# Optimization experiments

Hardware: AMD Instinct MI355X
Metric: run time of the kernel (lower is better)

Reference implementation:

```python
import jax, jax.numpy as jnp
import numpy as np

# Fixed canonical tree batching: complete binary tree, depth D, 2^D - 1 internal nodes.
O, P_, D = 64, 64, 6          # num_obs, num_particles, tree depth
H, OBS, SD, AD = 100, 100, 8, 10  # hidden, obs_emb, sample_emb, address_emb dims
IN = OBS + SD + AD            # GRUCell input dim = 118
N = 2 ** D - 1                # internal nodes per tree


def setup_inputs() -> dict:
    key = jax.random.key(0)
    ks = jax.random.split(key, 13)
    f = lambda k, s: jax.random.normal(k, s, dtype=jnp.float32)
    return {
        "obs_embeddings": f(ks[0], (O, OBS)),
        "sample_emb": f(ks[1], (O, P_, N, SD)),
        "addr_emb": f(ks[2], (O, P_, N, AD)),
        "W_ih": f(ks[3], (3 * H, IN)) * 0.1,
        "W_hh": f(ks[4], (3 * H, H)) * 0.1,
        "b_ih": f(ks[5], (3 * H,)) * 0.1,
        "b_hh": f(ks[6], (3 * H,)) * 0.1,
        "W1": f(ks[7], (50, H)) * 0.1,
        "b1": f(ks[8], (50,)) * 0.1,
        "W2": f(ks[9], (25, 50)) * 0.1,
        "b2": f(ks[10], (25,)) * 0.1,
        "W3": f(ks[11], (1, 25)) * 0.1,
        "b3": f(ks[12], (1,)) * 0.1,
    }


def reference(obs_embeddings, sample_emb, addr_emb, W_ih, W_hh, b_ih, b_hh,
              W1, b1, W2, b2, W3, b3):
    def gru_cell(x, h):
        # torch.nn.GRUCell math
        gi = x @ W_ih.T + b_ih
        gh = h @ W_hh.T + b_hh
        i_r, i_z, i_n = jnp.split(gi, 3, axis=-1)
        h_r, h_z, h_n = jnp.split(gh, 3, axis=-1)
        r = jax.nn.sigmoid(i_r + h_r)
        z = jax.nn.sigmoid(i_z + h_z)
        n = jnp.tanh(i_n + r * h_n)
        return (1.0 - z) * n + z * h

    # Leaves (terminals) contribute zero hidden state, per the torch code.
    h_child = jnp.zeros((O, P_, 2 ** (D - 1), H), dtype=sample_emb.dtype)
    h = h_child
    # Bottom-up over levels (root = level 0). Level l has 2^l nodes,
    # occupying flat indices [2^l - 1, 2^(l+1) - 2].
    for l in range(D - 1, -1, -1):
        w = 2 ** l
        s = w - 1
        obs_b = jnp.broadcast_to(obs_embeddings[:, None, None, :], (O, P_, w, OBS))
        x = jnp.concatenate(
            [obs_b, sample_emb[:, :, s:s + w], addr_emb[:, :, s:s + w]], axis=-1)
        h = gru_cell(x, h_child)  # [O, P_, w, H]
        if l > 0:
            # Parent hidden input = sum of its two children's embeddings.
            h_child = h.reshape(O, P_, w // 2, 2, H).sum(axis=3)
    root = h[:, :, 0, :]  # [O, P_, H]
    y = jax.nn.relu(root @ W1.T + b1)
    y = jax.nn.relu(y @ W2.T + b2)
    c = (y @ W3.T + b3)[..., 0]  # [O, P_]
    return jax.nn.logsumexp(c, axis=1) - jnp.log(jnp.float32(P_))
```

## Files before the change

### kernel.cpp

```cpp
#include <hip/hip_runtime.h>
#include <hip/hip_bf16.h>

typedef __attribute__((ext_vector_type(8))) short bf16x8;
typedef __attribute__((ext_vector_type(4))) float f32x4;

__device__ __forceinline__ float sigmoidf_(float x){ return 1.0f/(1.0f+__expf(-x)); }
__device__ __forceinline__ float tanhf_(float x){ return 1.0f - 2.0f/(1.0f+__expf(2.0f*x)); }
__device__ __forceinline__ unsigned short f2bf(float f){
    __hip_bfloat16 b = __float2bfloat16(f);
    return *reinterpret_cast<unsigned short*>(&b);
}
__device__ __forceinline__ float bf2f(unsigned short u){
    __hip_bfloat16 b = *reinterpret_cast<__hip_bfloat16*>(&u);
    return __bfloat162float(b);
}
__device__ __forceinline__ void gload_lds16(const void* gsrc, void* ldst){
    __builtin_amdgcn_global_load_lds(
        (const __attribute__((address_space(1))) unsigned int*)gsrc,
        (__attribute__((address_space(3))) unsigned int*)ldst,
        16, 0, 0);
}

__global__ __launch_bounds__(64) void precompute_kernel(
    const float* __restrict__ obs, const float* __restrict__ W_ih,
    const float* __restrict__ W_hh, const float* __restrict__ b_ih,
    const float* __restrict__ b_hh, const float* __restrict__ W1,
    const float* __restrict__ W2,
    unsigned short* __restrict__ Bg,
    float* __restrict__ W1T, float* __restrict__ W2T)
{
    int t = blockIdx.x * 64 + threadIdx.x;
    if (t < 688128) {
        int o = t / 10752, r = t % 10752;
        int s = r / 512, r2 = r % 512;
        int j = r2 / 32, kk = r2 % 32;
        int region = s / 7;
        int u = (s % 7) * 16 + j;
        unsigned short outv = 0;
        if (u < 100) {
            int gate = region * 100 + u;
            if (kk < 18) {
                outv = f2bf(W_ih[(size_t)gate * 118 + 100 + kk]);
            } else if (kk == 18 || kk == 19) {
                float bias = b_ih[gate] + (region < 2 ? b_hh[gate] : 0.f);
                const float* orow = obs + o * 100;
                const float* wrow = W_ih + (size_t)gate * 118;
                for (int k = 0; k < 100; ++k) bias = fmaf(orow[k], wrow[k], bias);
                if (kk == 18) outv = f2bf(bias);
                else          outv = f2bf(bias - bf2f(f2bf(bias)));
            }
        }
        int qr = kk >> 3, e = kk & 7;
        Bg[(size_t)o * 10752 + (size_t)((s * 4 + qr) * 16 + j) * 8 + e] = outv;
        return;
    }
    t -= 688128;
    if (t < 43008) {
        int ks = 1 + t / 10752, r = t % 10752;
        int s = r / 512, r2 = r % 512;
        int j = r2 / 32, kk = r2 % 32;
        int tt = (s < 14) ? s : s + 7;
        int region = tt / 7;
        int u = (tt % 7) * 16 + j;
        float wv = 0.f;
        if (u < 100) {
            int gate = (region == 3 ? 2 : region) * 100 + u;
            int kh = (ks - 1) * 32 + kk;
            if (kh < 100) wv = W_hh[(size_t)gate * 100 + kh];
        }
        int qr = kk >> 3, e = kk & 7;
        Bg[(size_t)688128 + (size_t)(ks - 1) * 10752
           + (size_t)((s * 4 + qr) * 16 + j) * 8 + e] = f2bf(wv);
        return;
    }
    t -= 43008;
    if (t < 512) {
        Bg[731136 + t] = 0;
        return;
    }
    t -= 512;
    if (t < 5000) { int g = t / 50, j = t % 50; W1T[t] = W1[j * 100 + g]; return; }
    t -= 5000;
    if (t < 1250) { int j = t / 25, i = t % 25; W2T[t] = W2[i * 50 + j]; }
}

template<int LW1, bool LEAF1, bool LAST>
__global__ __launch_bounds__(512) void fused_pair(
    const unsigned short* __restrict__ Bg,
    const float* __restrict__ bhh,
    const float* __restrict__ samp,
    const float* __restrict__ addr,
    const unsigned short* __restrict__ hin,
    unsigned short* __restrict__ hout)
{
    extern __shared__ unsigned short smem[];
    unsigned short* B0   = smem;
    unsigned short* BH   = smem + 10752;
    unsigned short* hmid = smem + 54272;

    const int tid = threadIdx.x;
    const int lane = tid & 63;
    const int wid = tid >> 6;
    const int j15 = lane & 15;
    const int qr = lane >> 4;
    const int wk = (blockIdx.x & 7) * (gridDim.x >> 3) + (blockIdx.x >> 3);
    const int c0 = wk * 128;
    const int c0w = c0 + wid * 16;
    const int o = c0 >> (LW1 + 6);

    {
        const char* g0 = (const char*)(Bg + (size_t)o * 10752);
        const char* gH = (const char*)(Bg + 688128);
        char* l0 = (char*)smem;
        #pragma unroll
        for (int it = 0; it < 13; ++it) {
            const int base = it * 512 + wid * 64;
            const int fi = base + lane;
            const char* src = (fi < 1344) ? g0 + (size_t)fi * 16
                                          : gH + (size_t)(fi - 1344) * 16;
            gload_lds16(src, l0 + (size_t)base * 16);
        }
        if (wid < 2) {
            const int base = 6656 + wid * 64;
            const int fi = base + lane;
            gload_lds16(gH + (size_t)(fi - 1344) * 16, l0 + (size_t)base * 16);
        }
    }

    f32x4 acc[28];
    #pragma unroll
    for (int t = 0; t < 28; ++t) acc[t] = (f32x4){0.f, 0.f, 0.f, 0.f};

    bf16x8 axhi, axlo;
    {
        const int w = 1 << LW1;
        const int cm = c0w + j15;
        const int opm = cm >> LW1;
        const int nodem = w - 1 + (cm & (w - 1));
        const size_t nb = (size_t)opm * 63 + nodem;
        float xv0=0.f,xv1=0.f,xv2=0.f,xv3=0.f,xv4=0.f,xv5=0.f,xv6=0.f,xv7=0.f;
        if (qr == 0) {
            const float4* s4 = (const float4*)(samp + nb * 8);
            float4 a = s4[0], b = s4[1];
            xv0=a.x; xv1=a.y; xv2=a.z; xv3=a.w; xv4=b.x; xv5=b.y; xv6=b.z; xv7=b.w;
        } else if (qr == 1) {
            const float2* a2 = (const float2*)(addr + nb * 10);
            float2 e0=a2[0], e1=a2[1], e2=a2[2], e3=a2[3];
            xv0=e0.x; xv1=e0.y; xv2=e1.x; xv3=e1.y; xv4=e2.x; xv5=e2.y; xv6=e3.x; xv7=e3.y;
        } else if (qr == 2) {
            xv0 = addr[nb * 10 + 8]; xv1 = addr[nb * 10 + 9];
            xv2 = 1.0f;
            xv3 = 1.0f;
        }
        #define CVT(e, val) { unsigned short hh = f2bf(val); \
            axhi[e] = (short)hh; axlo[e] = (short)f2bf((val) - bf2f(hh)); }
        CVT(0, xv0) CVT(1, xv1) CVT(2, xv2) CVT(3, xv3)
        CVT(4, xv4) CVT(5, xv5) CVT(6, xv6) CVT(7, xv7)
        #undef CVT
    }
    bf16x8 ah1[4];
    if constexpr (!LEAF1) {
        const size_t arow = (size_t)(c0w + j15) * 128 + qr * 8;
        #pragma unroll
        for (int m = 0; m < 4; ++m)
            ah1[m] = *(const bf16x8*)(hin + arow + m * 32);
    }
    __syncthreads();

    #pragma unroll
    for (int s = 0; s < 21; ++s) {
        bf16x8 bhi = *(const bf16x8*)(B0 + ((s * 4 + qr) * 16 + j15) * 8);
        acc[s] = __builtin_amdgcn_mfma_f32_16x16x32_bf16(axhi, bhi, acc[s], 0, 0, 0);
        acc[s] = __builtin_amdgcn_mfma_f32_16x16x32_bf16(axlo, bhi, acc[s], 0, 0, 0);
    }
    if constexpr (!LEAF1) {
        #pragma unroll
        for (int ks = 1; ks <= 4; ++ks) {
            const unsigned short* hp = BH + (ks - 1) * 10752;
            #pragma unroll
            for (int s = 0; s < 21; ++s) {
                const int d = (s < 14) ? s : s + 7;
                bf16x8 bhi = *(const bf16x8*)(hp + ((s * 4 + qr) * 16 + j15) * 8);
                acc[d] = __builtin_amdgcn_mfma_f32_16x16x32_bf16(ah1[ks - 1], bhi, acc[d], 0, 0, 0);
            }
        }
    }

    #pragma unroll
    for (int t = 0; t < 7; ++t) {
        const int u = t * 16 + j15;
        const float bh = (u < 100) ? bhh[200 + u] : 0.f;
        float hv0, hv1, hv2, hv3;
        #define GATE(reg, hvout) { \
            float rr = sigmoidf_(acc[t][reg]); \
            float zz = sigmoidf_(acc[t + 7][reg]); \
            float nn = tanhf_(acc[t + 14][reg] + rr * (acc[t + 21][reg] + bh)); \
            float hcv = 0.f; \
            if constexpr (!LEAF1) \
                hcv = bf2f(hin[(size_t)(c0w + qr * 4 + reg) * 128 + u]); \
            hvout = nn + zz * (hcv - nn); }
        GATE(0, hv0) GATE(1, hv1) GATE(2, hv2) GATE(3, hv3)
        #undef GATE
        const int r0 = wid * 8 + qr * 2;
        hmid[(r0)     * 136 + u] = f2bf(hv0 + hv1);
        hmid[(r0 + 1) * 136 + u] = f2bf(hv2 + hv3);
    }
    for (int f = tid; f < 1024; f += 512)
        hmid[(f >> 4) * 136 + 112 + (f & 15)] = 0;
    __syncthreads();

    {
        constexpr int LW2 = LW1 - 1;
        const int c20 = c0 >> 1;
        const int c2w = c20 + wid * 16;
        if (wid >= 4) return;

        #pragma unroll
        for (int t = 0; t < 28; ++t) acc[t] = (f32x4){0.f, 0.f, 0.f, 0.f};

        bf16x8 axhi2, axlo2;
        {
            const int w = 1 << LW2;
            const int cm = c2w + j15;
            const int opm = cm >> LW2;
            const int nodem = w - 1 + (cm & (w - 1));
            const size_t nb = (size_t)opm * 63 + nodem;
            float xv0=0.f,xv1=0.f,xv2=0.f,xv3=0.f,xv4=0.f,xv5=0.f,xv6=0.f,xv7=0.f;
            if (qr == 0) {
                const float4* s4 = (const float4*)(samp + nb * 8);
                float4 a = s4[0], b = s4[1];
                xv0=a.x; xv1=a.y; xv2=a.z; xv3=a.w; xv4=b.x; xv5=b.y; xv6=b.z; xv7=b.w;
            } else if (qr == 1) {
                const float2* a2 = (const float2*)(addr + nb * 10);
                float2 e0=a2[0], e1=a2[1], e2=a2[2], e3=a2[3];
                xv0=e0.x; xv1=e0.y; xv2=e1.x; xv3=e1.y; xv4=e2.x; xv5=e2.y; xv6=e3.x; xv7=e3.y;
            } else if (qr == 2) {
                xv0 = addr[nb * 10 + 8]; xv1 = addr[nb * 10 + 9];
                xv2 = 1.0f;
                xv3 = 1.0f;
            }
            #define CVT(e, val) { unsigned short hh = f2bf(val); \
                axhi2[e] = (short)hh; axlo2[e] = (short)f2bf((val) - bf2f(hh)); }
            CVT(0, xv0) CVT(1, xv1) CVT(2, xv2) CVT(3, xv3)
            CVT(4, xv4) CVT(5, xv5) CVT(6, xv6) CVT(7, xv7)
            #undef CVT
        }

        #pragma unroll
        for (int s = 0; s < 21; ++s) {
            bf16x8 bhi = *(const bf16x8*)(B0 + ((s * 4 + qr) * 16 + j15) * 8);
            acc[s] = __builtin_amdgcn_mfma_f32_16x16x32_bf16(axhi2, bhi, acc[s], 0, 0, 0);
            acc[s] = __builtin_amdgcn_mfma_f32_16x16x32_bf16(axlo2, bhi, acc[s], 0, 0, 0);
        }
        #pragma unroll
        for (int ks = 1; ks <= 4; ++ks) {
            bf16x8 ahi = *(const bf16x8*)(hmid + (wid * 16 + j15) * 136
                                               + (ks - 1) * 32 + qr * 8);
            const unsigned short* hp = BH + (ks - 1) * 10752;
            #pragma unroll
            for (int s = 0; s < 21; ++s) {
                const int d = (s < 14) ? s : s + 7;
                bf16x8 bhi = *(const bf16x8*)(hp + ((s * 4 + qr) * 16 + j15) * 8);
                acc[d] = __builtin_amdgcn_mfma_f32_16x16x32_bf16(ahi, bhi, acc[d], 0, 0, 0);
            }
        }

        #pragma unroll
        for (int t = 0; t < 7; ++t) {
            const int u = t * 16 + j15;
            const float bh = (u < 100) ? bhh[200 + u] : 0.f;
            float hv0, hv1, hv2, hv3;
            #define GATE(reg, hvout) { \
                float rr = sigmoidf_(acc[t][reg]); \
                float zz = sigmoidf_(acc[t + 7][reg]); \
                float nn = tanhf_(acc[t + 14][reg] + rr * (acc[t + 21][reg] + bh)); \
                float hcv = bf2f(hmid[(wid * 16 + qr * 4 + reg) * 136 + u]); \
                hvout = nn + zz * (hcv - nn); }
            GATE(0, hv0) GATE(1, hv1) GATE(2, hv2) GATE(3, hv3)
            #undef GATE
            if (LAST) {
                unsigned short* r0 = hout + (size_t)(c2w + qr * 4) * 128 + u;
                r0[0]   = f2bf(hv0);
                r0[128] = f2bf(hv1);
                r0[256] = f2bf(hv2);
                r0[384] = f2bf(hv3);
            } else {
                unsigned short* r0 = hout + (size_t)((c2w >> 1) + qr * 2) * 128 + u;
                r0[0]   = f2bf(hv0 + hv1);
                r0[128] = f2bf(hv2 + hv3);
            }
        }
        const int u2 = 112 + j15;
        if (LAST) {
            #pragma unroll
            for (int reg = 0; reg < 4; ++reg)
                hout[(size_t)(c2w + qr * 4 + reg) * 128 + u2] = 0;
        } else {
            #pragma unroll
            for (int p = 0; p < 2; ++p)
                hout[(size_t)((c2w >> 1) + qr * 2 + p) * 128 + u2] = 0;
        }
    }
}

__global__ __launch_bounds__(256) void mlp_lse(
    const unsigned short* __restrict__ h0,
    const float* __restrict__ W1T,
    const float* __restrict__ b1,
    const float* __restrict__ W2T,
    const float* __restrict__ b2,
    const float* __restrict__ W3,
    const float* __restrict__ b3,
    float* __restrict__ out)
{
    __shared__ float hs[64 * 101];
    __shared__ float w1s[5008];
    __shared__ float w2s[1250];
    __shared__ float y1s[64 * 50];

    const int o = blockIdx.x;
    const int tid = threadIdx.x;
    const int lane = tid & 63;
    const int wid = tid >> 6;

    for (int f = tid; f < 6400; f += 256) {
        int cl = f / 100, g = f - cl * 100;
        hs[cl * 101 + g] = bf2f(h0[(size_t)(o * 64 + cl) * 128 + g]);
    }
    for (int f = tid; f < 5000; f += 256) w1s[f] = W1T[f];
    for (int f = tid; f < 1250; f += 256) w2s[f] = W2T[f];
    __syncthreads();

    const int jbase = wid * 13;
    const int jn = (wid < 3) ? 13 : 11;
    float y1[13];
    #pragma unroll
    for (int jj = 0; jj < 13; ++jj) y1[jj] = b1[jbase + jj < 50 ? jbase + jj : 49];
    #pragma unroll 2
    for (int g = 0; g < 100; ++g) {
        float rg = hs[lane * 101 + g];
        const float* wr = w1s + g * 50 + jbase;
        #pragma unroll
        for (int jj = 0; jj < 13; ++jj) y1[jj] = fmaf(rg, wr[jj], y1[jj]);
    }
    #pragma unroll
    for (int jj = 0; jj < 13; ++jj)
        if (jj < jn) y1s[lane * 50 + jbase + jj] = y1[jj];
    __syncthreads();
    if (wid != 0) return;

    const int p = lane;
    float y2[25];
    #pragma unroll
    for (int i = 0; i < 25; ++i) y2[i] = b2[i];
    #pragma unroll 2
    for (int j = 0; j < 50; ++j) {
        float v = fmaxf(y1s[p * 50 + j], 0.0f);
        const float* wr = w2s + j * 25;
        #pragma unroll
        for (int i = 0; i < 25; ++i) y2[i] = fmaf(v, wr[i], y2[i]);
    }

    float cv = b3[0];
    #pragma unroll
    for (int i = 0; i < 25; ++i) cv = fmaf(fmaxf(y2[i], 0.0f), W3[i], cv);

    float m = cv;
    #pragma unroll
    for (int s = 1; s < 64; s <<= 1) m = fmaxf(m, __shfl_xor(m, s));
    float e = __expf(cv - m);
    #pragma unroll
    for (int s = 1; s < 64; s <<= 1) e += __shfl_xor(e, s);
    if (p == 0) out[o] = m + __logf(e) - 4.1588830833596715f;
}

extern "C" void kernel_launch(void* const* d_in, const int* in_sizes, int n_in,
                              void* d_out, int out_size, void* d_ws, size_t ws_size,
                              hipStream_t stream)
{
    const float* obs  = (const float*)d_in[0];
    const float* samp = (const float*)d_in[1];
    const float* addr = (const float*)d_in[2];
    const float* W_ih = (const float*)d_in[3];
    const float* W_hh = (const float*)d_in[4];
    const float* b_ih = (const float*)d_in[5];
    const float* b_hh = (const float*)d_in[6];
    const float* W1   = (const float*)d_in[7];
    const float* b1   = (const float*)d_in[8];
    const float* W2   = (const float*)d_in[9];
    const float* b2   = (const float*)d_in[10];
    const float* W3   = (const float*)d_in[11];
    const float* b3   = (const float*)d_in[12];
    float* out = (float*)d_out;

    float* ws = (float*)d_ws;
    unsigned short* Bg = (unsigned short*)ws;
    float* W1T = ws + 365824;
    float* W2T = ws + 370824;
    unsigned short* hU1 = (unsigned short*)(ws + 372080);
    unsigned short* hU2 = (unsigned short*)(ws + 2469232);
    unsigned short* hU3 = (unsigned short*)(ws + 2993520);

    const int DYN_LDS = 125952;
    (void)hipFuncSetAttribute((const void*)fused_pair<5, true, false>,
        hipFuncAttributeMaxDynamicSharedMemorySize, DYN_LDS);
    (void)hipFuncSetAttribute((const void*)fused_pair<3, false, false>,
        hipFuncAttributeMaxDynamicSharedMemorySize, DYN_LDS);
    (void)hipFuncSetAttribute((const void*)fused_pair<1, false, true>,
        hipFuncAttributeMaxDynamicSharedMemorySize, DYN_LDS);

    precompute_kernel<<<(737898 + 63) / 64, 64, 0, stream>>>(
        obs, W_ih, W_hh, b_ih, b_hh, W1, W2, Bg, W1T, W2T);

    fused_pair<5, true, false><<<1024, 512, DYN_LDS, stream>>>(
        Bg, b_hh, samp, addr, nullptr, hU1);
    fused_pair<3, false, false><<<256, 512, DYN_LDS, stream>>>(
        Bg, b_hh, samp, addr, hU1, hU2);
    fused_pair<1, false, true><<<64, 512, DYN_LDS, stream>>>(
        Bg, b_hh, samp, addr, hU2, hU3);

    mlp_lse<<<64, 256, 0, stream>>>(hU3, W1T, b1, W2T, b2, W3, b3, out);
}
```

Baseline: 132.7 us.

## Process two row chunks per block to amortize weight LDS staging

Each fused_pair block now loops over CHUNKS 128-row chunks for the first level, reusing the weight tiles staged in LDS, and then runs the second level over the combined half-rows using CHUNKS*4 waves. Grid sizes are halved for the first two launches, and LDS is sized to hold the larger intermediate buffer. This cuts repeated global-to-LDS weight loads per block but serializes the chunks inside a block and reduces the number of blocks available for parallelism.

After: 138.8 us. 1.05x slower.

```diff
diff --git a/kernel.cpp b/kernel.cpp
--- a/kernel.cpp
+++ b/kernel.cpp
@@ -84,7 +84,7 @@
     if (t < 1250) { int j = t / 25, i = t % 25; W2T[t] = W2[i * 50 + j]; }
 }
 
-template<int LW1, bool LEAF1, bool LAST>
+template<int LW1, bool LEAF1, bool LAST, int CHUNKS>
 __global__ __launch_bounds__(512) void fused_pair(
     const unsigned short* __restrict__ Bg,
     const float* __restrict__ bhh,
@@ -104,9 +104,8 @@
     const int j15 = lane & 15;
     const int qr = lane >> 4;
     const int wk = (blockIdx.x & 7) * (gridDim.x >> 3) + (blockIdx.x >> 3);
-    const int c0 = wk * 128;
-    const int c0w = c0 + wid * 16;
-    const int o = c0 >> (LW1 + 6);
+    const int blockBase = wk * (128 * CHUNKS);
+    const int o = blockBase >> (LW1 + 6);
 
     {
         const char* g0 = (const char*)(Bg + (size_t)o * 10752);
@@ -126,94 +125,101 @@
             gload_lds16(gH + (size_t)(fi - 1344) * 16, l0 + (size_t)base * 16);
         }
     }
+    __syncthreads();
 
     f32x4 acc[28];
-    #pragma unroll
-    for (int t = 0; t < 28; ++t) acc[t] = (f32x4){0.f, 0.f, 0.f, 0.f};
-
-    bf16x8 axhi, axlo;
-    {
-        const int w = 1 << LW1;
-        const int cm = c0w + j15;
-        const int opm = cm >> LW1;
-        const int nodem = w - 1 + (cm & (w - 1));
-        const size_t nb = (size_t)opm * 63 + nodem;
-        float xv0=0.f,xv1=0.f,xv2=0.f,xv3=0.f,xv4=0.f,xv5=0.f,xv6=0.f,xv7=0.f;
-        if (qr == 0) {
-            const float4* s4 = (const float4*)(samp + nb * 8);
-            float4 a = s4[0], b = s4[1];
-            xv0=a.x; xv1=a.y; xv2=a.z; xv3=a.w; xv4=b.x; xv5=b.y; xv6=b.z; xv7=b.w;
-        } else if (qr == 1) {
-            const float2* a2 = (const float2*)(addr + nb * 10);
-            float2 e0=a2[0], e1=a2[1], e2=a2[2], e3=a2[3];
-            xv0=e0.x; xv1=e0.y; xv2=e1.x; xv3=e1.y; xv4=e2.x; xv5=e2.y; xv6=e3.x; xv7=e3.y;
-        } else if (qr == 2) {
-            xv0 = addr[nb * 10 + 8]; xv1 = addr[nb * 10 + 9];
-            xv2 = 1.0f;
-            xv3 = 1.0f;
-        }
-        #define CVT(e, val) { unsigned short hh = f2bf(val); \
-            axhi[e] = (short)hh; axlo[e] = (short)f2bf((val) - bf2f(hh)); }
-        CVT(0, xv0) CVT(1, xv1) CVT(2, xv2) CVT(3, xv3)
-        CVT(4, xv4) CVT(5, xv5) CVT(6, xv6) CVT(7, xv7)
-        #undef CVT
-    }
-    bf16x8 ah1[4];
-    if constexpr (!LEAF1) {
-        const size_t arow = (size_t)(c0w + j15) * 128 + qr * 8;
-        #pragma unroll
-        for (int m = 0; m < 4; ++m)
-            ah1[m] = *(const bf16x8*)(hin + arow + m * 32);
-    }
-    __syncthreads();
-
-    #pragma unroll
-    for (int s = 0; s < 21; ++s) {
-        bf16x8 bhi = *(const bf16x8*)(B0 + ((s * 4 + qr) * 16 + j15) * 8);
-        acc[s] = __builtin_amdgcn_mfma_f32_16x16x32_bf16(axhi, bhi, acc[s], 0, 0, 0);
-        acc[s] = __builtin_amdgcn_mfma_f32_16x16x32_bf16(axlo, bhi, acc[s], 0, 0, 0);
-    }
-    if constexpr (!LEAF1) {
-        #pragma unroll
-        for (int ks = 1; ks <= 4; ++ks) {
-            const unsigned short* hp = BH + (ks - 1) * 10752;
+
+    #pragma unroll 1
+    for (int ch = 0; ch < CHUNKS; ++ch) {
+        const int c0 = blockBase + ch * 128;
+        const int c0w = c0 + wid * 16;
+
+        #pragma unroll
+        for (int t = 0; t < 28; ++t) acc[t] = (f32x4){0.f, 0.f, 0.f, 0.f};
+
+        bf16x8 axhi, axlo;
+        {
+            const int w = 1 << LW1;
+            const int cm = c0w + j15;
+            const int opm = cm >> LW1;
+            const int nodem = w - 1 + (cm & (w - 1));
+            const size_t nb = (size_t)opm * 63 + nodem;
+            float xv0=0.f,xv1=0.f,xv2=0.f,xv3=0.f,xv4=0.f,xv5=0.f,xv6=0.f,xv7=0.f;
+            if (qr == 0) {
+                const float4* s4 = (const float4*)(samp + nb * 8);
+                float4 a = s4[0], b = s4[1];
+                xv0=a.x; xv1=a.y; xv2=a.z; xv3=a.w; xv4=b.x; xv5=b.y; xv6=b.z; xv7=b.w;
+            } else if (qr == 1) {
+                const float2* a2 = (const float2*)(addr + nb * 10);
+                float2 e0=a2[0], e1=a2[1], e2=a2[2], e3=a2[3];
+                xv0=e0.x; xv1=e0.y; xv2=e1.x; xv3=e1.y; xv4=e2.x; xv5=e2.y; xv6=e3.x; xv7=e3.y;
+            } else if (qr == 2) {
+                xv0 = addr[nb * 10 + 8]; xv1 = addr[nb * 10 + 9];
+                xv2 = 1.0f;
+                xv3 = 1.0f;
+            }
+            #define CVT(e, val) { unsigned short hh = f2bf(val); \
+                axhi[e] = (short)hh; axlo[e] = (short)f2bf((val) - bf2f(hh)); }
+            CVT(0, xv0) CVT(1, xv1) CVT(2, xv2) CVT(3, xv3)
+            CVT(4, xv4) CVT(5, xv5) CVT(6, xv6) CVT(7, xv7)
+            #undef CVT
+        }
+        bf16x8 ah1[4];
+        if constexpr (!LEAF1) {
+            const size_t arow = (size_t)(c0w + j15) * 128 + qr * 8;
             #pragma unroll
-            for (int s = 0; s < 21; ++s) {
-                const int d = (s < 14) ? s : s + 7;
-                bf16x8 bhi = *(const bf16x8*)(hp + ((s * 4 + qr) * 16 + j15) * 8);
-                acc[d] = __builtin_amdgcn_mfma_f32_16x16x32_bf16(ah1[ks - 1], bhi, acc[d], 0, 0, 0);
-            }
-        }
-    }
-
-    #pragma unroll
-    for (int t = 0; t < 7; ++t) {
-        const int u = t * 16 + j15;
-        const float bh = (u < 100) ? bhh[200 + u] : 0.f;
-        float hv0, hv1, hv2, hv3;
-        #define GATE(reg, hvout) { \
-            float rr = sigmoidf_(acc[t][reg]); \
-            float zz = sigmoidf_(acc[t + 7][reg]); \
-            float nn = tanhf_(acc[t + 14][reg] + rr * (acc[t + 21][reg] + bh)); \
-            float hcv = 0.f; \
-            if constexpr (!LEAF1) \
-                hcv = bf2f(hin[(size_t)(c0w + qr * 4 + reg) * 128 + u]); \
-            hvout = nn + zz * (hcv - nn); }
-        GATE(0, hv0) GATE(1, hv1) GATE(2, hv2) GATE(3, hv3)
-        #undef GATE
-        const int r0 = wid * 8 + qr * 2;
-        hmid[(r0)     * 136 + u] = f2bf(hv0 + hv1);
-        hmid[(r0 + 1) * 136 + u] = f2bf(hv2 + hv3);
-    }
-    for (int f = tid; f < 1024; f += 512)
+            for (int m = 0; m < 4; ++m)
+                ah1[m] = *(const bf16x8*)(hin + arow + m * 32);
+        }
+
+        #pragma unroll
+        for (int s = 0; s < 21; ++s) {
+            bf16x8 bhi = *(const bf16x8*)(B0 + ((s * 4 + qr) * 16 + j15) * 8);
+            acc[s] = __builtin_amdgcn_mfma_f32_16x16x32_bf16(axhi, bhi, acc[s], 0, 0, 0);
+            acc[s] = __builtin_amdgcn_mfma_f32_16x16x32_bf16(axlo, bhi, acc[s], 0, 0, 0);
+        }
+        if constexpr (!LEAF1) {
+            #pragma unroll
+            for (int ks = 1; ks <= 4; ++ks) {
+                const unsigned short* hp = BH + (ks - 1) * 10752;
+                #pragma unroll
+                for (int s = 0; s < 21; ++s) {
+                    const int d = (s < 14) ? s : s + 7;
+                    bf16x8 bhi = *(const bf16x8*)(hp + ((s * 4 + qr) * 16 + j15) * 8);
+                    acc[d] = __builtin_amdgcn_mfma_f32_16x16x32_bf16(ah1[ks - 1], bhi, acc[d], 0, 0, 0);
+                }
+            }
+        }
+
+        #pragma unroll
+        for (int t = 0; t < 7; ++t) {
+            const int u = t * 16 + j15;
+            const float bh = (u < 100) ? bhh[200 + u] : 0.f;
+            float hv0, hv1, hv2, hv3;
+            #define GATE(reg, hvout) { \
+                float rr = sigmoidf_(acc[t][reg]); \
+                float zz = sigmoidf_(acc[t + 7][reg]); \
+                float nn = tanhf_(acc[t + 14][reg] + rr * (acc[t + 21][reg] + bh)); \
+                float hcv = 0.f; \
+                if constexpr (!LEAF1) \
+                    hcv = bf2f(hin[(size_t)(c0w + qr * 4 + reg) * 128 + u]); \
+                hvout = nn + zz * (hcv - nn); }
+            GATE(0, hv0) GATE(1, hv1) GATE(2, hv2) GATE(3, hv3)
+            #undef GATE
+            const int r0 = ch * 64 + wid * 8 + qr * 2;
+            hmid[(r0)     * 136 + u] = f2bf(hv0 + hv1);
+            hmid[(r0 + 1) * 136 + u] = f2bf(hv2 + hv3);
+        }
+    }
+    for (int f = tid; f < CHUNKS * 1024; f += 512)
         hmid[(f >> 4) * 136 + 112 + (f & 15)] = 0;
     __syncthreads();
 
     {
         constexpr int LW2 = LW1 - 1;
-        const int c20 = c0 >> 1;
+        if (wid >= CHUNKS * 4) return;
+        const int c20 = blockBase >> 1;
         const int c2w = c20 + wid * 16;
-        if (wid >= 4) return;
 
         #pragma unroll
         for (int t = 0; t < 28; ++t) acc[t] = (f32x4){0.f, 0.f, 0.f, 0.f};
@@ -401,22 +407,23 @@
     unsigned short* hU2 = (unsigned short*)(ws + 2469232);
     unsigned short* hU3 = (unsigned short*)(ws + 2993520);
 
-    const int DYN_LDS = 125952;
-    (void)hipFuncSetAttribute((const void*)fused_pair<5, true, false>,
-        hipFuncAttributeMaxDynamicSharedMemorySize, DYN_LDS);
-    (void)hipFuncSetAttribute((const void*)fused_pair<3, false, false>,
-        hipFuncAttributeMaxDynamicSharedMemorySize, DYN_LDS);
-    (void)hipFuncSetAttribute((const void*)fused_pair<1, false, true>,
-        hipFuncAttributeMaxDynamicSharedMemorySize, DYN_LDS);
+    const int LDS2 = (10752 + 43520 + 2 * 8704) * 2;
+    const int LDS1 = (10752 + 43520 + 1 * 8704) * 2;
+    (void)hipFuncSetAttribute((const void*)fused_pair<5, true, false, 2>,
+        hipFuncAttributeMaxDynamicSharedMemorySize, LDS2);
+    (void)hipFuncSetAttribute((const void*)fused_pair<3, false, false, 2>,
+        hipFuncAttributeMaxDynamicSharedMemorySize, LDS2);
+    (void)hipFuncSetAttribute((const void*)fused_pair<1, false, true, 1>,
+        hipFuncAttributeMaxDynamicSharedMemorySize, LDS1);
 
     precompute_kernel<<<(737898 + 63) / 64, 64, 0, stream>>>(
         obs, W_ih, W_hh, b_ih, b_hh, W1, W2, Bg, W1T, W2T);
 
-    fused_pair<5, true, false><<<1024, 512, DYN_LDS, stream>>>(
+    fused_pair<5, true, false, 2><<<512, 512, LDS2, stream>>>(
         Bg, b_hh, samp, addr, nullptr, hU1);
-    fused_pair<3, false, false><<<256, 512, DYN_LDS, stream>>>(
+    fused_pair<3, false, false, 2><<<128, 512, LDS2, stream>>>(
         Bg, b_hh, samp, addr, hU1, hU2);
-    fused_pair<1, false, true><<<64, 512, DYN_LDS, stream>>>(
+    fused_pair<1, false, true, 1><<<64, 512, LDS1, stream>>>(
         Bg, b_hh, samp, addr, hU2, hU3);
 
     mlp_lse<<<64, 256, 0, stream>>>(hU3, W1T, b1, W2T, b2, W3, b3, out);
```
